# Performance work log

Hardware: AMD Instinct MI355X
Metric: run time of the kernel (lower is better)

The kernel has to match this reference:

```python
import jax, jax.numpy as jnp
import numpy as np

B, S, HID = 2, 4096, 768
H, DH = 12, 64
FF = 3072
W = 128  # one-sided attention band; window span = 2*W+1
EPS = 1e-12


def _ln(x, g, b):
    m = jnp.mean(x, axis=-1, keepdims=True)
    v = jnp.var(x, axis=-1, keepdims=True)
    return (x - m) * jax.lax.rsqrt(v + EPS) * g + b


def _band_attend(q, k, v, dmask, w):
    # q,k,v: (B,H,S,D) fp32; dmask: (B,S,2w+1) additive key-mask. Returns (B,S,H,D).
    b, h, s, d = q.shape
    nc = s // w
    qc = q.reshape(b, h, nc, w, d)
    pad = ((0, 0), (0, 0), (w, w), (0, 0))
    kp = jnp.pad(k, pad)
    vp = jnp.pad(v, pad)
    win = jnp.arange(nc)[:, None] * w + jnp.arange(3 * w)[None, :]  # (nc, 3w) indices into padded seq
    kc = kp[:, :, win]  # (B,H,nc,3w,D)
    vc = vp[:, :, win]
    s3 = jnp.einsum('bhcxd,bhcyd->bhcxy', qc, kc)  # (B,H,nc,w,3w)
    # extract band: query i in chunk attends keys j in [i, i+2w] of the 3w window
    off = jnp.arange(w)[:, None] + jnp.arange(2 * w + 1)[None, :]  # (w, 2w+1)
    band = jnp.take_along_axis(s3, off[None, None, None], axis=-1)  # (B,H,nc,w,2w+1)
    band = band.reshape(b, h, s, 2 * w + 1)
    keypos = jnp.arange(s)[:, None] + jnp.arange(-w, w + 1)[None, :]
    valid = (keypos >= 0) & (keypos < s)  # mask_invalid_locations
    band = jnp.where(valid[None, None], band, -1e30)
    band = band + dmask[:, None]
    p = jax.nn.softmax(band, axis=-1)
    # scatter probs back to chunk-dense (w, 3w) layout for the PV matmul
    pc = p.reshape(b, h, nc, w, 2 * w + 1)
    j = jnp.arange(3 * w)[None, :] - jnp.arange(w)[:, None]  # (w,3w) offset indices
    ok = (j >= 0) & (j <= 2 * w)
    jcl = jnp.clip(j, 0, 2 * w)
    pdense = jnp.take_along_axis(pc, jcl[None, None, None], axis=-1)  # (B,H,nc,w,3w)
    pdense = jnp.where(ok[None, None, None], pdense, 0.0)
    ctx = jnp.einsum('bhcxy,bhcyd->bhcxd', pdense, vc)  # (B,H,nc,w,D)
    return ctx.reshape(b, h, s, d).transpose(0, 2, 1, 3)


def setup_inputs() -> dict:
    key = jax.random.key(0)
    ks = jax.random.split(key, 8)
    sc = 0.02
    inp = {
        'hidden_states': jax.random.normal(ks[0], (B, S, HID), jnp.float32),
        'attention_mask': jax.random.randint(ks[1], (B, 1, 1, S), 0, 2, jnp.int32),
        'Wq': jax.random.normal(ks[2], (HID, HID), jnp.float32) * sc,
        'bq': jnp.zeros((HID,), jnp.float32),
        'Wk': jax.random.normal(ks[3], (HID, HID), jnp.float32) * sc,
        'bk': jnp.zeros((HID,), jnp.float32),
        'Wv': jax.random.normal(ks[4], (HID, HID), jnp.float32) * sc,
        'bv': jnp.zeros((HID,), jnp.float32),
        'Wd': jax.random.normal(ks[5], (HID, HID), jnp.float32) * sc,
        'bd': jnp.zeros((HID,), jnp.float32),
        'ln1_g': jnp.ones((HID,), jnp.float32),
        'ln1_b': jnp.zeros((HID,), jnp.float32),
        'Wf': jax.random.normal(ks[6], (HID, FF), jnp.float32) * sc,
        'bf': jnp.zeros((FF,), jnp.float32),
        'Wo': jax.random.normal(ks[7], (FF, HID), jnp.float32) * sc,
        'bo': jnp.zeros((HID,), jnp.float32),
        'ln2_g': jnp.ones((HID,), jnp.float32),
        'ln2_b': jnp.zeros((HID,), jnp.float32),
    }
    return inp


def reference(hidden_states, attention_mask, Wq, bq, Wk, bk, Wv, bv, Wd, bd,
              ln1_g, ln1_b, Wf, bf, Wo, bo, ln2_g, ln2_b):
    def heads(x):
        return x.reshape(B, S, H, DH).transpose(0, 2, 1, 3)  # (B,H,S,DH)

    q = heads(hidden_states @ Wq + bq).astype(jnp.float32) / np.float32(np.sqrt(DH))
    k = heads(hidden_states @ Wk + bk).astype(jnp.float32)
    v = heads(hidden_states @ Wv + bv).astype(jnp.float32)

    am = attention_mask.reshape(B, S)
    maskvals = jnp.where(am != 0, -10000.0, 0.0).astype(jnp.float32)  # (B,S)
    mpad = jnp.pad(maskvals, ((0, 0), (W, W)))
    kidx = jnp.arange(S)[:, None] + jnp.arange(2 * W + 1)[None, :]
    dmask = mpad[:, kidx]  # (B,S,2w+1)

    ctx = _band_attend(q, k, v, dmask, W)  # (B,S,H,DH)

    w_d = Wd.reshape(H, DH, HID)
    proj = jnp.einsum('bfnd,ndh->bfh', ctx, w_d) + bd
    attn_out = _ln(hidden_states + proj, ln1_g, ln1_b)

    ff = jax.nn.gelu(attn_out @ Wf + bf, approximate=False)
    ff = ff @ Wo + bo
    return _ln(ff + attn_out, ln2_g, ln2_b)
```

## Files before the change

kernel.cpp:

```cpp
#include <hip/hip_runtime.h>
#include <cstdint>
#include <cstddef>

#define S_LEN 4096
#define HIDD 768
#define NH 12
#define FFD 3072

typedef float f32x4 __attribute__((ext_vector_type(4)));
typedef short s16x8 __attribute__((ext_vector_type(8)));
typedef short s16x4 __attribute__((ext_vector_type(4)));

__device__ __forceinline__ short f2bf(float f) {
  unsigned u = __float_as_uint(f);
  u += 0x7fffu + ((u >> 16) & 1u);
  return (short)(u >> 16);
}
__device__ __forceinline__ float bf2f(short s) {
  return __uint_as_float(((unsigned)(unsigned short)s) << 16);
}

__device__ __forceinline__ void gload16(const short* g, short* l) {
  __builtin_amdgcn_global_load_lds(
      (__attribute__((address_space(1))) void*)(void*)const_cast<short*>(g),
      (__attribute__((address_space(3))) void*)l, 16, 0, 0);
}

__global__ void prep_k(const float* __restrict__ x, short* __restrict__ xo,
                       const float* __restrict__ Wq, const float* __restrict__ Wk,
                       const float* __restrict__ Wv, const float* __restrict__ Wd,
                       const float* __restrict__ Wf, const float* __restrict__ Wo,
                       short* __restrict__ oq, short* __restrict__ ok_,
                       short* __restrict__ ov, short* __restrict__ od,
                       short* __restrict__ of_, short* __restrict__ oo) {
  __shared__ float tl[64][65];
  int id = blockIdx.x;
  if (id < 6144) {
    size_t i = (size_t)id * 256 + threadIdx.x;
    float4 f = ((const float4*)x)[i];
    s16x4 v;
    v[0] = f2bf(f.x); v[1] = f2bf(f.y); v[2] = f2bf(f.z); v[3] = f2bf(f.w);
    ((s16x4*)xo)[i] = v;
    return;
  }
  id -= 6144;
  const float* in; short* out; int R, C, tr, tc;
  if (id < 576) {
    int wsel = id / 144; int t = id % 144; tr = t / 12; tc = t % 12; R = 768; C = 768;
    in = wsel == 0 ? Wq : wsel == 1 ? Wk : wsel == 2 ? Wv : Wd;
    out = wsel == 0 ? oq : wsel == 1 ? ok_ : wsel == 2 ? ov : od;
  } else if (id < 1152) {
    int t = id - 576; tr = t / 48; tc = t % 48; R = 768; C = 3072; in = Wf; out = of_;
  } else {
    int t = id - 1152; tr = t / 12; tc = t % 12; R = 3072; C = 768; in = Wo; out = oo;
  }
  int r0 = tr * 64, c0 = tc * 64;
  int tid = threadIdx.x;
  #pragma unroll
  for (int i = 0; i < 16; i++) {
    int idx = i * 256 + tid; int r = idx >> 6, cc = idx & 63;
    tl[r][cc] = in[(size_t)(r0 + r) * C + c0 + cc];
  }
  __syncthreads();
  #pragma unroll
  for (int i = 0; i < 16; i++) {
    int idx = i * 256 + tid; int cc = idx >> 6, rr = idx & 63;
    out[(size_t)(c0 + cc) * R + r0 + rr] = f2bf(tl[rr][cc]);
  }
}

__global__ void vtrans_k(const short* __restrict__ vh, short* __restrict__ vth) {
  __shared__ short tl[64][72];
  int s0 = blockIdx.x * 64; int bh = blockIdx.y;
  int tid = threadIdx.x;
  const short* base = vh + ((size_t)bh << 18);
  #pragma unroll
  for (int i = 0; i < 16; i++) {
    int idx = i * 256 + tid; int r = idx >> 6, cc = idx & 63;
    tl[r][cc] = base[(size_t)(s0 + r) * 64 + cc];
  }
  __syncthreads();
  short* ob = vth + ((size_t)bh << 18);
  #pragma unroll
  for (int i = 0; i < 16; i++) {
    int idx = i * 256 + tid; int dh = idx >> 6, s = idx & 63;
    ob[((size_t)dh << 12) + s0 + s] = tl[s][dh];
  }
}

template <int EPI, int BN>
__global__ void __launch_bounds__(256) gemm_bt(
    const short* __restrict__ A, const short* __restrict__ Bt,
    const float* __restrict__ bias, const float* __restrict__ bias1,
    const float* __restrict__ bias2, const void* __restrict__ resid,
    void* __restrict__ out, int N, int K) {
  constexpr int NT = BN / 32;
  __shared__ __align__(16) short As[2][128 * 64];
  __shared__ __align__(16) short Bs[2][BN * 64];
  const int tid = threadIdx.x;
  const int lane = tid & 63;
  const int w = tid >> 6;
  const int wr = w >> 1, wc = w & 1;
  const int m0 = blockIdx.x * 128, n0 = blockIdx.y * BN;
  const int lr = lane >> 3;
  const int seg = (lane & 7) ^ lr;
  f32x4 acc[4][NT];
  #pragma unroll
  for (int i = 0; i < 4; i++)
    #pragma unroll
    for (int j = 0; j < NT; j++) { acc[i][j][0] = 0.f; acc[i][j][1] = 0.f; acc[i][j][2] = 0.f; acc[i][j][3] = 0.f; }

  const short* Ab = A + (size_t)(m0 + lr) * K + seg * 8;
  const short* Bb = Bt + (size_t)(n0 + lr) * K + seg * 8;

  auto stage = [&](int buf, int k0) {
    #pragma unroll
    for (int i = 0; i < 4; i++) {
      const int ca = w * 4 + i;
      gload16(Ab + (size_t)(ca * 8) * K + k0, &As[buf][ca * 512]);
    }
    #pragma unroll
    for (int i = 0; i < NT; i++) {
      const int cb = w * NT + i;
      gload16(Bb + (size_t)(cb * 8) * K + k0, &Bs[buf][cb * 512]);
    }
  };

  const int nt_k = K >> 6;
  stage(0, 0);
  int cur = 0;
  for (int t = 0; t < nt_k; ++t) {
    const bool more = (t + 1 < nt_k);
    if (more) stage(cur ^ 1, (t + 1) << 6);
    if (more) {
      if constexpr (NT == 4) asm volatile("s_waitcnt vmcnt(8)" ::: "memory");
      else                   asm volatile("s_waitcnt vmcnt(6)" ::: "memory");
    } else {
      asm volatile("s_waitcnt vmcnt(0)" ::: "memory");
    }
    __builtin_amdgcn_s_barrier();
    __builtin_amdgcn_sched_barrier(0);
    const int kc = (lane >> 4) * 8;
    #pragma unroll
    for (int ks = 0; ks < 2; ks++) {
      const int kb = ks * 32 + kc;
      s16x8 af[4], bfr[NT];
      #pragma unroll
      for (int mt = 0; mt < 4; mt++) {
        const int arow = wr * 64 + mt * 16 + (lane & 15);
        af[mt] = *(const s16x8*)&As[cur][arow * 64 + (kb ^ ((arow & 7) << 3))];
      }
      #pragma unroll
      for (int nt = 0; nt < NT; nt++) {
        const int brow = wc * (BN / 2) + nt * 16 + (lane & 15);
        bfr[nt] = *(const s16x8*)&Bs[cur][brow * 64 + (kb ^ ((brow & 7) << 3))];
      }
      #pragma unroll
      for (int mt = 0; mt < 4; mt++)
        #pragma unroll
        for (int nt = 0; nt < NT; nt++)
          acc[mt][nt] = __builtin_amdgcn_mfma_f32_16x16x32_bf16(af[mt], bfr[nt], acc[mt][nt], 0, 0, 0);
    }
    if (more) {
      __builtin_amdgcn_sched_barrier(0);
      __builtin_amdgcn_s_barrier();
      cur ^= 1;
    }
  }
  #pragma unroll
  for (int nt = 0; nt < NT; nt++) {
    const int col = n0 + wc * (BN / 2) + nt * 16 + (lane & 15);
    if (EPI == 0) {
      const int cwhich = col >= 1536 ? 2 : (col >= 768 ? 1 : 0);
      const int cwi = col - cwhich * 768;
      const float* bsel = cwhich == 0 ? bias : (cwhich == 1 ? bias1 : bias2);
      const float bvv = bsel[cwi];
      const float sc = (cwhich == 0) ? 0.125f : 1.f;
      const int hh = cwi >> 6, dh = cwi & 63;
      short* outp = (short*)out + (size_t)cwhich * ((size_t)8192 * 768);
      #pragma unroll
      for (int mt = 0; mt < 4; mt++) {
        #pragma unroll
        for (int rr = 0; rr < 4; rr++) {
          const int row = m0 + wr * 64 + mt * 16 + (lane >> 4) * 4 + rr;
          const int b = row >> 12, s = row & 4095;
          outp[((((size_t)b * NH + hh) * S_LEN + s) << 6) + dh] = f2bf((acc[mt][nt][rr] + bvv) * sc);
        }
      }
    } else {
      const float bvv = bias[col];
      #pragma unroll
      for (int mt = 0; mt < 4; mt++) {
        #pragma unroll
        for (int rr = 0; rr < 4; rr++) {
          const int row = m0 + wr * 64 + mt * 16 + (lane >> 4) * 4 + rr;
          float v = acc[mt][nt][rr] + bvv;
          if (EPI == 1) {
            float u = 0.7978845608f * v * (1.f + 0.044715f * v * v);
            float e = __expf(2.f * u);
            float th = 1.f - 2.f / (e + 1.f);
            ((short*)out)[(size_t)row * N + col] = f2bf(0.5f * v * (1.f + th));
          } else if (EPI == 2) {
            ((float*)out)[(size_t)row * N + col] = v + ((const float*)resid)[(size_t)row * N + col];
          } else {
            ((float*)out)[(size_t)row * N + col] = v + bf2f(((const short*)resid)[(size_t)row * N + col]);
          }
        }
      }
    }
  }
}

__global__ void __launch_bounds__(512, 1) attn_k(
    const short* __restrict__ qh, const short* __restrict__ kh,
    const short* __restrict__ vth, const int* __restrict__ am,
    short* __restrict__ ctx) {
  extern __shared__ char smraw[];
  short* Kb = (short*)smraw;
  float* dmw = (float*)(smraw + 55296);
  short* Pb = (short*)(smraw + 56832);
  const int c = blockIdx.x;
  const int bh = blockIdx.y;
  const int b = bh / NH, hh = bh % NH;
  const int tid = threadIdx.x, lane = tid & 63, w = tid >> 6;
  const int q0 = c * 128, kw0 = q0 - 128;

  for (int ch = tid; ch < 3072; ch += 512) {
    int n = ch >> 3, seg = ch & 7;
    int kp = kw0 + n; kp = kp < 0 ? 0 : (kp > S_LEN - 1 ? S_LEN - 1 : kp);
    *(s16x8*)&Kb[n * 72 + seg * 8] = *(const s16x8*)&kh[(((size_t)bh * S_LEN + kp) << 6) + seg * 8];
  }
  for (int n = tid; n < 384; n += 512) {
    int kp = kw0 + n;
    float d;
    if (kp < 0 || kp >= S_LEN) d = -1e30f;
    else d = (am[b * S_LEN + kp] != 0) ? -10000.f : 0.f;
    dmw[n] = d;
  }
  __syncthreads();

  const short* qrow = qh + ((((size_t)bh * S_LEN) + q0 + w * 16 + (lane & 15)) << 6);
  s16x8 aq0 = *(const s16x8*)&qrow[(lane >> 4) * 8];
  s16x8 aq1 = *(const s16x8*)&qrow[32 + (lane >> 4) * 8];

  f32x4 sacc[24];
  #pragma unroll
  for (int t = 0; t < 24; t++) { sacc[t][0] = 0.f; sacc[t][1] = 0.f; sacc[t][2] = 0.f; sacc[t][3] = 0.f; }
  #pragma unroll
  for (int t = 0; t < 24; t++) {
    const short* kr = &Kb[(t * 16 + (lane & 15)) * 72 + (lane >> 4) * 8];
    s16x8 bk0 = *(const s16x8*)&kr[0];
    s16x8 bk1 = *(const s16x8*)&kr[32];
    sacc[t] = __builtin_amdgcn_mfma_f32_16x16x32_bf16(aq0, bk0, sacc[t], 0, 0, 0);
    sacc[t] = __builtin_amdgcn_mfma_f32_16x16x32_bf16(aq1, bk1, sacc[t], 0, 0, 0);
  }
  const int mbase = w * 16 + (lane >> 4) * 4;
  #pragma unroll
  for (int t = 0; t < 24; t++) {
    int n = t * 16 + (lane & 15);
    float d = dmw[n];
    #pragma unroll
    for (int r = 0; r < 4; r++) {
      int j = n - (mbase + r);
      float sv = sacc[t][r] + d;
      if (j < 0 || j > 256) sv = -1e30f;
      sacc[t][r] = sv;
    }
  }
  short* Pw = Pb + w * 16 * 392;
  #pragma unroll
  for (int r = 0; r < 4; r++) {
    float mx = -3e38f;
    #pragma unroll
    for (int t = 0; t < 24; t++) mx = fmaxf(mx, sacc[t][r]);
    #pragma unroll
    for (int d = 1; d < 16; d <<= 1) mx = fmaxf(mx, __shfl_xor(mx, d));
    float sum = 0.f;
    #pragma unroll
    for (int t = 0; t < 24; t++) { float p = __expf(sacc[t][r] - mx); sacc[t][r] = p; sum += p; }
    #pragma unroll
    for (int d = 1; d < 16; d <<= 1) sum += __shfl_xor(sum, d);
    float inv = 1.f / sum;
    #pragma unroll
    for (int t = 0; t < 24; t++)
      Pw[((lane >> 4) * 4 + r) * 392 + t * 16 + (lane & 15)] = f2bf(sacc[t][r] * inv);
  }
  __syncthreads();

  short* Vt = (short*)smraw;
  for (int ch = tid; ch < 3072; ch += 512) {
    int dh = ch / 48, seg = ch % 48;
    int n0 = seg * 8, kp0 = kw0 + n0;
    const short* vr = vth + (((size_t)bh * 64 + dh) << 12);
    s16x8 vv;
    if (kp0 >= 0 && kp0 + 7 < S_LEN) {
      vv = *(const s16x8*)&vr[kp0];
    } else {
      #pragma unroll
      for (int e = 0; e < 8; e++) {
        int kp = kp0 + e; kp = kp < 0 ? 0 : (kp > S_LEN - 1 ? S_LEN - 1 : kp);
        vv[e] = vr[kp];
      }
    }
    *(s16x8*)&Vt[dh * 392 + n0] = vv;
  }
  __syncthreads();

  f32x4 oacc[4];
  #pragma unroll
  for (int i = 0; i < 4; i++) { oacc[i][0] = 0.f; oacc[i][1] = 0.f; oacc[i][2] = 0.f; oacc[i][3] = 0.f; }
  #pragma unroll
  for (int ksp = 0; ksp < 12; ksp++) {
    s16x8 pa = *(const s16x8*)&Pw[(lane & 15) * 392 + ksp * 32 + (lane >> 4) * 8];
    #pragma unroll
    for (int ct = 0; ct < 4; ct++) {
      s16x8 vb = *(const s16x8*)&Vt[(ct * 16 + (lane & 15)) * 392 + ksp * 32 + (lane >> 4) * 8];
      oacc[ct] = __builtin_amdgcn_mfma_f32_16x16x32_bf16(pa, vb, oacc[ct], 0, 0, 0);
    }
  }
  #pragma unroll
  for (int ct = 0; ct < 4; ct++) {
    #pragma unroll
    for (int r = 0; r < 4; r++) {
      int srow = q0 + w * 16 + (lane >> 4) * 4 + r;
      int col = hh * 64 + ct * 16 + (lane & 15);
      ctx[((size_t)b * S_LEN + srow) * HIDD + col] = f2bf(oacc[ct][r]);
    }
  }
}

template <int OUTBF>
__global__ void ln_k(const float* __restrict__ in, const float* __restrict__ g,
                     const float* __restrict__ bb, void* __restrict__ out) {
  int row = blockIdx.x * 4 + (threadIdx.x >> 6);
  int lane = threadIdx.x & 63;
  const float4* x = (const float4*)(in + (size_t)row * HIDD);
  float4 v0 = x[lane], v1 = x[lane + 64], v2 = x[lane + 128];
  float s = v0.x + v0.y + v0.z + v0.w + v1.x + v1.y + v1.z + v1.w + v2.x + v2.y + v2.z + v2.w;
  float ss = v0.x * v0.x + v0.y * v0.y + v0.z * v0.z + v0.w * v0.w
           + v1.x * v1.x + v1.y * v1.y + v1.z * v1.z + v1.w * v1.w
           + v2.x * v2.x + v2.y * v2.y + v2.z * v2.z + v2.w * v2.w;
  #pragma unroll
  for (int d = 1; d < 64; d <<= 1) { s += __shfl_xor(s, d); ss += __shfl_xor(ss, d); }
  float mean = s * (1.f / 768.f);
  float var = ss * (1.f / 768.f) - mean * mean;
  float rs = rsqrtf(var + 1e-12f);
  const float4* gp = (const float4*)g;
  const float4* bp = (const float4*)bb;
  #pragma unroll
  for (int seg = 0; seg < 3; seg++) {
    int idx = lane + seg * 64;
    float4 vv = seg == 0 ? v0 : seg == 1 ? v1 : v2;
    float4 gg = gp[idx], b4 = bp[idx];
    float o0 = (vv.x - mean) * rs * gg.x + b4.x;
    float o1 = (vv.y - mean) * rs * gg.y + b4.y;
    float o2 = (vv.z - mean) * rs * gg.z + b4.z;
    float o3 = (vv.w - mean) * rs * gg.w + b4.w;
    if (OUTBF) {
      s16x4 o; o[0] = f2bf(o0); o[1] = f2bf(o1); o[2] = f2bf(o2); o[3] = f2bf(o3);
      ((s16x4*)out)[(size_t)row * 192 + idx] = o;
    } else {
      float4 o; o.x = o0; o.y = o1; o.z = o2; o.w = o3;
      ((float4*)out)[(size_t)row * 192 + idx] = o;
    }
  }
}

extern "C" void kernel_launch(void* const* d_in, const int* in_sizes, int n_in,
                              void* d_out, int out_size, void* d_ws, size_t ws_size,
                              hipStream_t stream) {
  const float* hid = (const float*)d_in[0];
  const int* am = (const int*)d_in[1];
  const float* Wq = (const float*)d_in[2];  const float* bq = (const float*)d_in[3];
  const float* Wk = (const float*)d_in[4];  const float* bk = (const float*)d_in[5];
  const float* Wv = (const float*)d_in[6];  const float* bv = (const float*)d_in[7];
  const float* Wd = (const float*)d_in[8];  const float* bd = (const float*)d_in[9];
  const float* g1 = (const float*)d_in[10]; const float* b1 = (const float*)d_in[11];
  const float* Wf = (const float*)d_in[12]; const float* bf = (const float*)d_in[13];
  const float* Wo = (const float*)d_in[14]; const float* bo = (const float*)d_in[15];
  const float* g2 = (const float*)d_in[16]; const float* b2 = (const float*)d_in[17];

  char* ws = (char*)d_ws;
  size_t off = 0;
  auto alloc = [&](size_t bytes) { char* p = ws + off; off += (bytes + 255) & ~(size_t)255; return p; };
  short* Xb   = (short*)alloc((size_t)8192 * 768 * 2);
  short* Wqb  = (short*)alloc((size_t)768 * 768 * 2);
  short* Wkb  = (short*)alloc((size_t)768 * 768 * 2);
  short* Wvb  = (short*)alloc((size_t)768 * 768 * 2);
  short* Wdb  = (short*)alloc((size_t)768 * 768 * 2);
  short* Wfb  = (short*)alloc((size_t)3072 * 768 * 2);
  short* Wob  = (short*)alloc((size_t)768 * 3072 * 2);
  short* qh   = (short*)alloc((size_t)8192 * 768 * 2);
  short* kh   = (short*)alloc((size_t)8192 * 768 * 2);
  short* vh   = (short*)alloc((size_t)8192 * 768 * 2);
  short* vth  = (short*)alloc((size_t)8192 * 768 * 2);
  short* ctx  = (short*)alloc((size_t)8192 * 768 * 2);
  short* aob  = (short*)alloc((size_t)8192 * 768 * 2);
  short* ffb  = (short*)alloc((size_t)8192 * 3072 * 2);
  float* f2r  = (float*)alloc((size_t)8192 * 768 * 4);
  float* ln1in = (float*)d_out;
  (void)kh; (void)vh;

  hipFuncSetAttribute(reinterpret_cast<const void*>(attn_k),
                      hipFuncAttributeMaxDynamicSharedMemorySize, 157184);

  prep_k<<<7872, 256, 0, stream>>>(hid, Xb, Wq, Wk, Wv, Wd, Wf, Wo,
                                   Wqb, Wkb, Wvb, Wdb, Wfb, Wob);

  gemm_bt<0, 128><<<dim3(64, 18), 256, 0, stream>>>(Xb, Wqb, bq, bk, bv, nullptr, qh, 2304, 768);
  vtrans_k<<<dim3(64, 24), 256, 0, stream>>>(vh, vth);
  attn_k<<<dim3(32, 24), 512, 157184, stream>>>(qh, kh, vth, am, ctx);
  gemm_bt<2, 64><<<dim3(64, 12), 256, 0, stream>>>(ctx, Wdb, bd, nullptr, nullptr, hid, ln1in, 768, 768);
  ln_k<1><<<2048, 256, 0, stream>>>(ln1in, g1, b1, aob);
  gemm_bt<1, 128><<<dim3(64, 24), 256, 0, stream>>>(aob, Wfb, bf, nullptr, nullptr, nullptr, ffb, 3072, 768);
  gemm_bt<3, 64><<<dim3(64, 12), 256, 0, stream>>>(ffb, Wob, bo, nullptr, nullptr, aob, f2r, 768, 3072);
  ln_k<0><<<2048, 256, 0, stream>>>(f2r, g2, b2, d_out);
}
```

Measured before the change: 259.8 us.

## Add single-buffered 128x256 wide GEMM for QKV and FFN-up, simplify bt pipeline

Adds a gemm_wide kernel with 128x256 tiles, where each wave owns a 128x64 output slab. It uses a single LDS buffer and precomputed swizzled offsets. This kernel now runs the QKV projection and the FFN-up GEMM with GELU, aiming for more operand reuse per LDS load and fewer blocks. The remaining gemm_bt drops its manual vmcnt waits and s_barrier in favour of plain __syncthreads around the double buffer, and its unused epilogues are removed. The wide kernel's single buffer means loads no longer overlap compute, and the larger tile raises register pressure and gives fewer blocks (576 and 768) across the CUs.

```diff
diff --git a/kernel.cpp b/kernel.cpp
--- a/kernel.cpp
+++ b/kernel.cpp
@@ -88,11 +88,125 @@
   }
 }
 
+template <int EPI>
+__global__ void __launch_bounds__(256) gemm_wide(
+    const short* __restrict__ A, const short* __restrict__ Bt,
+    const float* __restrict__ bias, const float* __restrict__ bias1,
+    const float* __restrict__ bias2, void* __restrict__ out, int N, int K) {
+  __shared__ __align__(16) short As[128 * 64];
+  __shared__ __align__(16) short Bs[256 * 64];
+  const int tid = threadIdx.x;
+  const int lane = tid & 63;
+  const int w = tid >> 6;
+  const int lm = lane & 15, lk = lane >> 4;
+  const int m0 = blockIdx.x * 128, n0 = blockIdx.y * 256;
+  const int lr = lane >> 3;
+  const int seg = (lane & 7) ^ lr;
+
+  f32x4 acc[8][4];
+  #pragma unroll
+  for (int i = 0; i < 8; i++)
+    #pragma unroll
+    for (int j = 0; j < 4; j++) { acc[i][j][0] = 0.f; acc[i][j][1] = 0.f; acc[i][j][2] = 0.f; acc[i][j][3] = 0.f; }
+
+  const short* aG[4]; short* aL[4];
+  #pragma unroll
+  for (int i = 0; i < 4; i++) {
+    const int c = w * 4 + i;
+    aG[i] = A + (size_t)(m0 + c * 8 + lr) * K + seg * 8;
+    aL[i] = &As[c * 512];
+  }
+  const short* bG[8]; short* bL[8];
+  #pragma unroll
+  for (int i = 0; i < 8; i++) {
+    const int c = w * 8 + i;
+    bG[i] = Bt + (size_t)(n0 + c * 8 + lr) * K + seg * 8;
+    bL[i] = &Bs[c * 512];
+  }
+
+  const int kc = lk * 8;
+  int aoffs[8][2], boffs[4][2];
+  #pragma unroll
+  for (int mt = 0; mt < 8; mt++) {
+    const int arow = mt * 16 + lm;
+    #pragma unroll
+    for (int ks = 0; ks < 2; ks++)
+      aoffs[mt][ks] = arow * 64 + ((ks * 32 + kc) ^ ((arow & 7) << 3));
+  }
+  #pragma unroll
+  for (int nt = 0; nt < 4; nt++) {
+    const int brow = w * 64 + nt * 16 + lm;
+    #pragma unroll
+    for (int ks = 0; ks < 2; ks++)
+      boffs[nt][ks] = brow * 64 + ((ks * 32 + kc) ^ ((brow & 7) << 3));
+  }
+
+  const int nt_k = K >> 6;
+  for (int t = 0; t < nt_k; ++t) {
+    const int k0 = t << 6;
+    #pragma unroll
+    for (int i = 0; i < 4; i++) gload16(aG[i] + k0, aL[i]);
+    #pragma unroll
+    for (int i = 0; i < 8; i++) gload16(bG[i] + k0, bL[i]);
+    __syncthreads();
+    #pragma unroll
+    for (int ks = 0; ks < 2; ks++) {
+      s16x8 af[8], bfr[4];
+      #pragma unroll
+      for (int mt = 0; mt < 8; mt++) af[mt] = *(const s16x8*)&As[aoffs[mt][ks]];
+      #pragma unroll
+      for (int nt = 0; nt < 4; nt++) bfr[nt] = *(const s16x8*)&Bs[boffs[nt][ks]];
+      #pragma unroll
+      for (int mt = 0; mt < 8; mt++)
+        #pragma unroll
+        for (int nt = 0; nt < 4; nt++)
+          acc[mt][nt] = __builtin_amdgcn_mfma_f32_16x16x32_bf16(af[mt], bfr[nt], acc[mt][nt], 0, 0, 0);
+    }
+    if (t + 1 < nt_k) __syncthreads();
+  }
+
+  #pragma unroll
+  for (int nt = 0; nt < 4; nt++) {
+    const int col = n0 + w * 64 + nt * 16 + lm;
+    if (EPI == 0) {
+      const int cwhich = col >= 1536 ? 2 : (col >= 768 ? 1 : 0);
+      const int cwi = col - cwhich * 768;
+      const float* bsel = cwhich == 0 ? bias : (cwhich == 1 ? bias1 : bias2);
+      const float bvv = bsel[cwi];
+      const float sc = (cwhich == 0) ? 0.125f : 1.f;
+      const int hh = cwi >> 6, dh = cwi & 63;
+      short* outp = (short*)out + (size_t)cwhich * ((size_t)8192 * 768);
+      #pragma unroll
+      for (int mt = 0; mt < 8; mt++) {
+        #pragma unroll
+        for (int rr = 0; rr < 4; rr++) {
+          const int row = m0 + mt * 16 + lk * 4 + rr;
+          const int b = row >> 12, s = row & 4095;
+          outp[((((size_t)b * NH + hh) * S_LEN + s) << 6) + dh] = f2bf((acc[mt][nt][rr] + bvv) * sc);
+        }
+      }
+    } else {
+      const float bvv = bias[col];
+      #pragma unroll
+      for (int mt = 0; mt < 8; mt++) {
+        #pragma unroll
+        for (int rr = 0; rr < 4; rr++) {
+          const int row = m0 + mt * 16 + lk * 4 + rr;
+          float v = acc[mt][nt][rr] + bvv;
+          float u = 0.7978845608f * v * (1.f + 0.044715f * v * v);
+          float e = __expf(2.f * u);
+          float th = 1.f - 2.f / (e + 1.f);
+          ((short*)out)[(size_t)row * N + col] = f2bf(0.5f * v * (1.f + th));
+        }
+      }
+    }
+  }
+}
+
 template <int EPI, int BN>
 __global__ void __launch_bounds__(256) gemm_bt(
     const short* __restrict__ A, const short* __restrict__ Bt,
-    const float* __restrict__ bias, const float* __restrict__ bias1,
-    const float* __restrict__ bias2, const void* __restrict__ resid,
+    const float* __restrict__ bias, const void* __restrict__ resid,
     void* __restrict__ out, int N, int K) {
   constexpr int NT = BN / 32;
   __shared__ __align__(16) short As[2][128 * 64];
@@ -128,18 +242,10 @@
 
   const int nt_k = K >> 6;
   stage(0, 0);
+  __syncthreads();
   int cur = 0;
   for (int t = 0; t < nt_k; ++t) {
-    const bool more = (t + 1 < nt_k);
-    if (more) stage(cur ^ 1, (t + 1) << 6);
-    if (more) {
-      if constexpr (NT == 4) asm volatile("s_waitcnt vmcnt(8)" ::: "memory");
-      else                   asm volatile("s_waitcnt vmcnt(6)" ::: "memory");
-    } else {
-      asm volatile("s_waitcnt vmcnt(0)" ::: "memory");
-    }
-    __builtin_amdgcn_s_barrier();
-    __builtin_amdgcn_sched_barrier(0);
+    if (t + 1 < nt_k) stage(cur ^ 1, (t + 1) << 6);
     const int kc = (lane >> 4) * 8;
     #pragma unroll
     for (int ks = 0; ks < 2; ks++) {
@@ -161,50 +267,22 @@
         for (int nt = 0; nt < NT; nt++)
           acc[mt][nt] = __builtin_amdgcn_mfma_f32_16x16x32_bf16(af[mt], bfr[nt], acc[mt][nt], 0, 0, 0);
     }
-    if (more) {
-      __builtin_amdgcn_sched_barrier(0);
-      __builtin_amdgcn_s_barrier();
-      cur ^= 1;
-    }
+    if (t + 1 < nt_k) { __syncthreads(); cur ^= 1; }
   }
   #pragma unroll
   for (int nt = 0; nt < NT; nt++) {
     const int col = n0 + wc * (BN / 2) + nt * 16 + (lane & 15);
-    if (EPI == 0) {
-      const int cwhich = col >= 1536 ? 2 : (col >= 768 ? 1 : 0);
-      const int cwi = col - cwhich * 768;
-      const float* bsel = cwhich == 0 ? bias : (cwhich == 1 ? bias1 : bias2);
-      const float bvv = bsel[cwi];
-      const float sc = (cwhich == 0) ? 0.125f : 1.f;
-      const int hh = cwi >> 6, dh = cwi & 63;
-      short* outp = (short*)out + (size_t)cwhich * ((size_t)8192 * 768);
-      #pragma unroll
-      for (int mt = 0; mt < 4; mt++) {
-        #pragma unroll
-        for (int rr = 0; rr < 4; rr++) {
-          const int row = m0 + wr * 64 + mt * 16 + (lane >> 4) * 4 + rr;
-          const int b = row >> 12, s = row & 4095;
-          outp[((((size_t)b * NH + hh) * S_LEN + s) << 6) + dh] = f2bf((acc[mt][nt][rr] + bvv) * sc);
-        }
-      }
-    } else {
-      const float bvv = bias[col];
-      #pragma unroll
-      for (int mt = 0; mt < 4; mt++) {
-        #pragma unroll
-        for (int rr = 0; rr < 4; rr++) {
-          const int row = m0 + wr * 64 + mt * 16 + (lane >> 4) * 4 + rr;
-          float v = acc[mt][nt][rr] + bvv;
-          if (EPI == 1) {
-            float u = 0.7978845608f * v * (1.f + 0.044715f * v * v);
-            float e = __expf(2.f * u);
-            float th = 1.f - 2.f / (e + 1.f);
-            ((short*)out)[(size_t)row * N + col] = f2bf(0.5f * v * (1.f + th));
-          } else if (EPI == 2) {
-            ((float*)out)[(size_t)row * N + col] = v + ((const float*)resid)[(size_t)row * N + col];
-          } else {
-            ((float*)out)[(size_t)row * N + col] = v + bf2f(((const short*)resid)[(size_t)row * N + col]);
-          }
+    const float bvv = bias[col];
+    #pragma unroll
+    for (int mt = 0; mt < 4; mt++) {
+      #pragma unroll
+      for (int rr = 0; rr < 4; rr++) {
+        const int row = m0 + wr * 64 + mt * 16 + (lane >> 4) * 4 + rr;
+        float v = acc[mt][nt][rr] + bvv;
+        if (EPI == 2) {
+          ((float*)out)[(size_t)row * N + col] = v + ((const float*)resid)[(size_t)row * N + col];
+        } else {
+          ((float*)out)[(size_t)row * N + col] = v + bf2f(((const short*)resid)[(size_t)row * N + col]);
         }
       }
     }
@@ -407,12 +485,12 @@
   prep_k<<<7872, 256, 0, stream>>>(hid, Xb, Wq, Wk, Wv, Wd, Wf, Wo,
                                    Wqb, Wkb, Wvb, Wdb, Wfb, Wob);
 
-  gemm_bt<0, 128><<<dim3(64, 18), 256, 0, stream>>>(Xb, Wqb, bq, bk, bv, nullptr, qh, 2304, 768);
+  gemm_wide<0><<<dim3(64, 9), 256, 0, stream>>>(Xb, Wqb, bq, bk, bv, qh, 2304, 768);
   vtrans_k<<<dim3(64, 24), 256, 0, stream>>>(vh, vth);
   attn_k<<<dim3(32, 24), 512, 157184, stream>>>(qh, kh, vth, am, ctx);
-  gemm_bt<2, 64><<<dim3(64, 12), 256, 0, stream>>>(ctx, Wdb, bd, nullptr, nullptr, hid, ln1in, 768, 768);
+  gemm_bt<2, 64><<<dim3(64, 12), 256, 0, stream>>>(ctx, Wdb, bd, hid, ln1in, 768, 768);
   ln_k<1><<<2048, 256, 0, stream>>>(ln1in, g1, b1, aob);
-  gemm_bt<1, 128><<<dim3(64, 24), 256, 0, stream>>>(aob, Wfb, bf, nullptr, nullptr, nullptr, ffb, 3072, 768);
-  gemm_bt<3, 64><<<dim3(64, 12), 256, 0, stream>>>(ffb, Wob, bo, nullptr, nullptr, aob, f2r, 768, 3072);
+  gemm_wide<1><<<dim3(64, 12), 256, 0, stream>>>(aob, Wfb, bf, nullptr, nullptr, ffb, 3072, 768);
+  gemm_bt<3, 64><<<dim3(64, 12), 256, 0, stream>>>(ffb, Wob, bo, aob, f2r, 768, 3072);
   ln_k<0><<<2048, 256, 0, stream>>>(f2r, g2, b2, d_out);
 }
```

New measurement: 321.7 us. 23.8% more time.
